# Kernel tuning notes

Measured on AMD Instinct MI355X. Metric: run time of the kernel, lower is better.

The kernel has to match this reference:

```python
import jax, jax.numpy as jnp
import numpy as np
import math

H, W = 1024, 1024

def setup_inputs() -> dict:
    key = jax.random.key(0)
    img = jax.random.uniform(key, (H, W), dtype=jnp.float32) * 255.0
    return {"InputImage": img}

def _phase_congruency(img):
    nrows, ncols = img.shape
    minWaveLength, mult = 3.0, 2.1
    nscale, norient = 5, 6
    sigmaOnf, k, cutOff, g = 0.55, 2.0, 0.5, 10.0
    eps = 1e-4

    cy, cx = nrows // 2, ncols // 2
    yy, xx = jnp.mgrid[0:nrows, 0:ncols]
    yy = (yy - cy) / nrows
    xx = (xx - cx) / ncols
    radius = jnp.sqrt(xx ** 2 + yy ** 2)
    radius = radius.at[cy, cx].set(1.0)
    theta = jnp.arctan2(-yy, xx)
    sintheta, costheta = jnp.sin(theta), jnp.cos(theta)

    # low-pass Butterworth (order 15, cutoff 0.45)
    normradius = radius / (jnp.abs(xx).max() * 2)
    lowpass = 1.0 / (1.0 + (normradius / 0.45) ** 30)

    # log-Gabor radial filters, [nscale, H, W]
    s = jnp.arange(nscale, dtype=jnp.float32)
    fo = 1.0 / (minWaveLength * mult ** s)            # [S]
    logGabor = jnp.exp(-jnp.log(radius[None] * (1.0 / fo)[:, None, None]) ** 2
                       / (2 * math.log(sigmaOnf) ** 2))
    annular = logGabor * lowpass[None]
    annular = annular.at[:, cy, cx].set(0.0)

    # angular spread, [norient, H, W]
    angl = jnp.arange(norient, dtype=jnp.float32) * (math.pi / norient)
    cosA, sinA = jnp.cos(angl), jnp.sin(angl)
    ds = sintheta[None] * cosA[:, None, None] - costheta[None] * sinA[:, None, None]
    dc = costheta[None] * cosA[:, None, None] + sintheta[None] * sinA[:, None, None]
    dtheta = jnp.minimum(jnp.abs(jnp.arctan2(ds, dc)) * (norient / 2), math.pi)
    spread = (jnp.cos(dtheta) + 1.0) / 2.0

    # full filter bank [O, S, H, W], shifted to DFT layout
    filt = jnp.fft.ifftshift(spread[:, None] * annular[None], axes=(-2, -1))

    F = jnp.fft.fft2(img)                              # complex64
    # cv2.idft is unscaled -> multiply numpy-style ifft by N
    z = jnp.fft.ifft2(filt * F[None, None]) * (nrows * ncols)   # [O,S,H,W]
    # original code: E (even) = channel 1 = Im(z), O (odd) = channel 0 = Re(z)
    E, O = z.imag, z.real
    An = jnp.abs(z)

    sumE = E.sum(axis=1)        # [O,H,W]
    sumO = O.sum(axis=1)
    sumAn = An.sum(axis=1)
    maxAn = An.max(axis=1)
    tau = jnp.median(An[:, 0].reshape(norient, -1), axis=1) / math.sqrt(math.log(4.0))

    XEnergy = jnp.sqrt(sumE ** 2 + sumO ** 2) + eps
    MeanE = sumE / XEnergy
    MeanO = sumO / XEnergy
    Energy = (E * MeanE[:, None] + O * MeanO[:, None]
              - jnp.abs(E * MeanO[:, None] - O * MeanE[:, None])).sum(axis=1)

    totalTau = tau * (1 - (1 / mult) ** nscale) / (1 - 1 / mult)   # [O]
    T = totalTau * math.sqrt(math.pi / 2) + k * totalTau * math.sqrt((4 - math.pi) / 2)
    Energy = jnp.maximum(Energy - T[:, None, None], 0.0)

    width = (sumAn / (maxAn + eps) - 1.0) / (nscale - 1)
    weight = 1.0 / (1.0 + jnp.exp((cutOff - width) * g))
    PC = weight * Energy / sumAn                       # [O,H,W]

    covx = PC * cosA[:, None, None]
    covy = PC * sinA[:, None, None]
    covx2 = (covx ** 2).sum(axis=0) / (norient / 2)
    covy2 = (covy ** 2).sum(axis=0) / (norient / 2)
    covxy = 4.0 * (covx * covy).sum(axis=0) / norient
    denom = jnp.sqrt(covxy ** 2 + (covx2 - covy2) ** 2) + eps
    M = (covy2 + covx2 + denom) / 2.0
    m = (covy2 + covx2 - denom) / 2.0
    return M, m

def reference(InputImage):
    M, m = _phase_congruency(InputImage)
    return (M, m)
```

## Files before the change

### kernel.cpp

```cpp
#include <hip/hip_runtime.h>
#include <math.h>

typedef float2 c2;

#define CSTR 1058
#define POS(n) (33*((n)>>5) + ((n)&31))

__device__ __forceinline__ c2 cmul(c2 a, c2 b){
  return make_float2(a.x*b.x - a.y*b.y, a.x*b.y + a.y*b.x);
}

__constant__ float2 c_tw32[16] = {
  {1.0f, 0.0f},
  {0.980785280f, 0.195090322f},
  {0.923879533f, 0.382683432f},
  {0.831469612f, 0.555570233f},
  {0.707106781f, 0.707106781f},
  {0.555570233f, 0.831469612f},
  {0.382683432f, 0.923879533f},
  {0.195090322f, 0.980785280f},
  {0.0f, 1.0f},
  {-0.195090322f, 0.980785280f},
  {-0.382683432f, 0.923879533f},
  {-0.555570233f, 0.831469612f},
  {-0.707106781f, 0.707106781f},
  {-0.831469612f, 0.555570233f},
  {-0.923879533f, 0.382683432f},
  {-0.980785280f, 0.195090322f}
};

__constant__ float c_lnfo[5]  = {1.0986123f, 1.8405496f, 2.5824700f, 3.3244106f, 4.0663219f};
__constant__ float c_angl[6]  = {0.0f, 0.5235988f, 1.0471976f, 1.5707963f, 2.0943951f, 2.6179939f};
__constant__ float c_cosA[6] = {1.0f, 0.8660254038f, 0.5f, 6.123233996e-17f, -0.5f, -0.8660254038f};
__constant__ float c_sinA[6] = {0.0f, 0.5f, 0.8660254038f, 1.0f, 0.8660254038f, 0.5f};

__device__ __forceinline__ constexpr int rev5(int k){
  return ((k&1)<<4) | ((k&2)<<2) | (k&4) | ((k&8)>>2) | ((k>>4)&1);
}

template<int SIGN, int M>
__device__ __forceinline__ void stage32(c2* r){
#pragma unroll
  for (int g = 0; g < 32; g += 2*M){
#pragma unroll
    for (int i = 0; i < M; ++i){
      const c2 a = r[g+i], b = r[g+i+M];
      r[g+i] = make_float2(a.x+b.x, a.y+b.y);
      c2 d = make_float2(a.x-b.x, a.y-b.y);
      if (i != 0){
        const float2 tt = c_tw32[i*(16/M)];
        d = cmul(d, make_float2(tt.x, (float)SIGN*tt.y));
      }
      r[g+i+M] = d;
    }
  }
}

template<int SIGN>
__device__ __forceinline__ void fft32(c2* r){
  stage32<SIGN,16>(r);
  stage32<SIGN,8>(r);
  stage32<SIGN,4>(r);
  stage32<SIGN,2>(r);
  stage32<SIGN,1>(r);
}

template<int SIGN>
__device__ void fft1024_4step(c2* slab, int t){
  const int sub = t & 7;
  const int idx = t >> 3;
  c2* line = slab + sub*CSTR;
  c2 r[32];
#pragma unroll
  for (int a = 0; a < 32; ++a) r[a] = line[33*a + idx];
  fft32<SIGN>(r);
  {
    const float ang = (float)SIGN * 0.006135923151542565f * (float)idx;
    c2 wst; sincosf(ang, &wst.y, &wst.x);
    c2 wc = make_float2(1.f, 0.f);
#pragma unroll
    for (int d = 0; d < 32; ++d){
      if ((d & 7) == 0 && d != 0){ float s, c; sincosf(ang*(float)d, &s, &c); wc = make_float2(c, s); }
      c2 v = r[rev5(d)];
      if (d != 0) v = cmul(v, wc);
      line[33*d + idx] = v;
      wc = cmul(wc, wst);
    }
  }
  __syncthreads();
#pragma unroll
  for (int b = 0; b < 32; ++b) r[b] = line[33*idx + b];
  __syncthreads();
  fft32<SIGN>(r);
#pragma unroll
  for (int c = 0; c < 32; ++c) line[33*c + idx] = r[rev5(c)];
}


template<int SIGN>
__global__ __launch_bounds__(256, 2) void k_col_fft(c2* __restrict__ Z){
  __shared__ c2 slab[8*CSTR];
  const int t = threadIdx.x;
  c2* base = Z + (size_t)blockIdx.y * 1048576;
  const int col0 = blockIdx.x * 8;
  const int cl = t & 7, rw = t >> 3;
#pragma unroll
  for (int it = 0; it < 32; ++it){
    const int row = it*32 + rw;
    slab[cl*CSTR + 33*it + rw] = base[(size_t)row*1024 + col0 + cl];
  }
  __syncthreads();
  fft1024_4step<SIGN>(slab, t);
  __syncthreads();
#pragma unroll
  for (int it = 0; it < 32; ++it){
    const int row = it*32 + rw;
    base[(size_t)row*1024 + col0 + cl] = slab[cl*CSTR + 33*it + rw];
  }
}

__global__ __launch_bounds__(256, 2) void k_row_fft_real(const float* __restrict__ in, c2* __restrict__ out){
  __shared__ c2 slab[8*CSTR];
  const int t = threadIdx.x;
  const int row0 = blockIdx.x * 8;
#pragma unroll
  for (int it = 0; it < 32; ++it){
    const int g = it*256 + t;
    const int r = g >> 10, n = g & 1023;
    slab[r*CSTR + POS(n)] = make_float2(in[(size_t)(row0+r)*1024 + n], 0.f);
  }
  __syncthreads();
  fft1024_4step<-1>(slab, t);
  __syncthreads();
#pragma unroll
  for (int it = 0; it < 32; ++it){
    const int g = it*256 + t;
    const int r = g >> 10, n = g & 1023;
    out[(size_t)(row0+r)*1024 + n] = slab[r*CSTR + POS(n)];
  }
}

__global__ __launch_bounds__(256, 2) void k_row_ifft_filter(const c2* __restrict__ F, c2* __restrict__ Z,
                                                            const float* __restrict__ lnrT,
                                                            const float* __restrict__ thetaT, int slot0){
  __shared__ c2 slab[8*CSTR];
  const int t = threadIdx.x;
  const int gslot = slot0 + blockIdx.y;
  const int orient = gslot / 5, scale = gslot - orient*5;
  const float lnfo = c_lnfo[scale], angl = c_angl[orient];
  const int row0 = blockIdx.x * 8;
  c2* dst = Z + (size_t)blockIdx.y * 1048576;
#pragma unroll
  for (int it = 0; it < 32; ++it){
    const int g = it*256 + t;
    const int r = g >> 10, n = g & 1023;
    const size_t gi = (size_t)(row0+r)*1024 + n;
    const c2 v = F[gi];
    const float lnr = lnrT[gi], th = thetaT[gi];
    const float u = lnr + lnfo;
    const float lg = __expf(-u*u*1.3989572f);
    const float lp = 1.0f/(1.0f + __expf(fmaf(30.f, lnr, 23.955231f)));
    float d = th - angl;
    if (d <= -3.14159274f) d += 6.28318548f;
    const float dth = fminf(fabsf(d)*3.0f, 3.14159274f);
    const float f = lg*lp*0.5f*(__cosf(dth)+1.0f);
    slab[r*CSTR + POS(n)] = make_float2(v.x*f, v.y*f);
  }
  __syncthreads();
  fft1024_4step<1>(slab, t);
  __syncthreads();
#pragma unroll
  for (int it = 0; it < 32; ++it){
    const int g = it*256 + t;
    const int r = g >> 10, n = g & 1023;
    dst[(size_t)(row0+r)*1024 + n] = slab[r*CSTR + POS(n)];
  }
}

__global__ __launch_bounds__(256) void k_filt_tab(float* __restrict__ lnrT, float* __restrict__ thetaT){
  const int r = blockIdx.x;
  const int t = threadIdx.x;
  const float yy = (float)(r < 512 ? r : r - 1024) * (1.0f/1024.0f);
#pragma unroll
  for (int j = 0; j < 4; ++j){
    const int c = t + 256*j;
    const float xx = (float)(c < 512 ? c : c - 1024) * (1.0f/1024.0f);
    const float radius = sqrtf(xx*xx + yy*yy);
    float lnr = logf(radius);
    if (r == 0 && c == 0) lnr = __int_as_float(0x7F800000);
    lnrT[r*1024 + c] = lnr;
    thetaT[r*1024 + c] = atan2f(-yy, xx);
  }
}


__device__ __forceinline__ unsigned amp_bits(const c2 v){
  return __float_as_uint(sqrtf(v.x*v.x + v.y*v.y));
}

__global__ __launch_bounds__(256) void k_med_p1b(const c2* __restrict__ Zb, size_t oStride,
                                                 unsigned* __restrict__ g1, int oBase){
  __shared__ unsigned h[4][4096];
  const int t = threadIdx.x;
  const int wv = t >> 6;
  const c2* z0 = Zb + (size_t)blockIdx.y * oStride;
  unsigned* gg = g1 + (size_t)(oBase + blockIdx.y) * 4096;
  for (int j = t; j < 4*4096; j += 256) ((unsigned*)h)[j] = 0;
  __syncthreads();
  const int base = blockIdx.x * 16384;
  for (int it = 0; it < 64; ++it){
    const unsigned bits = amp_bits(z0[base + it*256 + t]);
    atomicAdd(&h[wv][bits >> 20], 1u);
  }
  __syncthreads();
  for (int j = t; j < 4096; j += 256){
    const unsigned s = h[0][j] + h[1][j] + h[2][j] + h[3][j];
    if (s) atomicAdd(&gg[j], s);
  }
}

__global__ __launch_bounds__(256) void k_sel1b(const unsigned* __restrict__ g1,
                                               unsigned* __restrict__ sc1,
                                               unsigned* __restrict__ g2, int oBase){
  __shared__ unsigned partial[256];
  const int t = threadIdx.x;
  const int oo = oBase + blockIdx.x;
  const unsigned* gg = g1 + (size_t)oo * 4096;
  unsigned loc[16]; unsigned s = 0;
#pragma unroll
  for (int j = 0; j < 16; ++j){ loc[j] = gg[t*16 + j]; s += loc[j]; }
  partial[t] = s;
  __syncthreads();
  unsigned p = 0;
  for (int u = 0; u < t; ++u) p += partial[u];
  for (int which = 0; which < 2; ++which){
    const unsigned R = 524287u + (unsigned)which;
    if (R >= p && R - p < s){
      unsigned cum = p;
      for (int j = 0; j < 16; ++j){
        if (R - cum < loc[j]){ sc1[oo*4 + which*2] = (unsigned)(t*16 + j); sc1[oo*4 + which*2+1] = R - cum; break; }
        cum += loc[j];
      }
    }
  }
  for (int j = t; j < 8192; j += 256) g2[(size_t)oo*8192 + j] = 0;
}

__global__ __launch_bounds__(256) void k_med_p2b(const c2* __restrict__ Zb, size_t oStride,
                                                 const unsigned* __restrict__ sc1,
                                                 unsigned* __restrict__ g2, int oBase){
  __shared__ unsigned h[2][4096];
  const int t = threadIdx.x;
  const int oo = oBase + blockIdx.y;
  const c2* z0 = Zb + (size_t)blockIdx.y * oStride;
  unsigned* gg = g2 + (size_t)oo * 8192;
  for (int j = t; j < 8192; j += 256) ((unsigned*)h)[j] = 0;
  __syncthreads();
  const unsigned b0 = sc1[oo*4 + 0], b1 = sc1[oo*4 + 2];
  const int base = blockIdx.x * 16384;
  for (int it = 0; it < 64; ++it){
    const unsigned bits = amp_bits(z0[base + it*256 + t]);
    const unsigned top = bits >> 20;
    const unsigned mid = (bits >> 8) & 4095u;
    if (top == b0)      atomicAdd(&h[0][mid], 1u);
    else if (top == b1) atomicAdd(&h[1][mid], 1u);
  }
  __syncthreads();
  for (int j = t; j < 4096; j += 256){
    if (h[0][j]) atomicAdd(&gg[j], h[0][j]);
    if (h[1][j]) atomicAdd(&gg[4096 + j], h[1][j]);
  }
}

__global__ __launch_bounds__(256) void k_sel2b(const unsigned* __restrict__ g2,
                                               const unsigned* __restrict__ sc1,
                                               unsigned* __restrict__ sc2,
                                               unsigned* __restrict__ g3, int oBase){
  __shared__ unsigned partial[256];
  const int t = threadIdx.x;
  const int oo = oBase + blockIdx.x;
  const unsigned b0 = sc1[oo*4+0], lr0 = sc1[oo*4+1], b1 = sc1[oo*4+2], lr1 = sc1[oo*4+3];
  for (int which = 0; which < 2; ++which){
    const unsigned* hh = g2 + (size_t)oo*8192 + ((which == 1 && b1 != b0) ? 4096 : 0);
    const unsigned R = which ? lr1 : lr0;
    unsigned loc[16]; unsigned s = 0;
#pragma unroll
    for (int j = 0; j < 16; ++j){ loc[j] = hh[t*16 + j]; s += loc[j]; }
    partial[t] = s;
    __syncthreads();
    unsigned p = 0;
    for (int u = 0; u < t; ++u) p += partial[u];
    if (R >= p && R - p < s){
      unsigned cum = p;
      for (int j = 0; j < 16; ++j){
        if (R - cum < loc[j]){ sc2[oo*4 + which*2] = (unsigned)(t*16 + j); sc2[oo*4 + which*2+1] = R - cum; break; }
        cum += loc[j];
      }
    }
    __syncthreads();
  }
  for (int j = t; j < 512; j += 256) g3[(size_t)oo*512 + j] = 0;
}

__global__ __launch_bounds__(256) void k_med_p3b(const c2* __restrict__ Zb, size_t oStride,
                                                 const unsigned* __restrict__ sc1,
                                                 const unsigned* __restrict__ sc2,
                                                 unsigned* __restrict__ g3, int oBase){
  __shared__ unsigned h[2][256];
  const int t = threadIdx.x;
  const int oo = oBase + blockIdx.y;
  const c2* z0 = Zb + (size_t)blockIdx.y * oStride;
  unsigned* gg = g3 + (size_t)oo * 512;
  h[0][t] = 0; h[1][t] = 0;
  __syncthreads();
  const unsigned k0 = (sc1[oo*4+0] << 12) | sc2[oo*4+0];
  const unsigned k1 = (sc1[oo*4+2] << 12) | sc2[oo*4+2];
  const int base = blockIdx.x * 16384;
  for (int it = 0; it < 64; ++it){
    const unsigned bits = amp_bits(z0[base + it*256 + t]);
    const unsigned key = bits >> 8;
    if (key == k0)       atomicAdd(&h[0][bits & 255u], 1u);
    else if (key == k1)  atomicAdd(&h[1][bits & 255u], 1u);
  }
  __syncthreads();
  if (h[0][t]) atomicAdd(&gg[t], h[0][t]);
  if (h[1][t]) atomicAdd(&gg[256 + t], h[1][t]);
}

__global__ __launch_bounds__(256) void k_sel3b(const unsigned* __restrict__ g3,
                                               const unsigned* __restrict__ sc1,
                                               const unsigned* __restrict__ sc2,
                                               float* __restrict__ Tval, int oBase){
  __shared__ unsigned partial[256];
  __shared__ float vres[2];
  const int t = threadIdx.x;
  const int oo = oBase + blockIdx.x;
  const unsigned k0 = (sc1[oo*4+0] << 12) | sc2[oo*4+0];
  const unsigned k1 = (sc1[oo*4+2] << 12) | sc2[oo*4+2];
  for (int which = 0; which < 2; ++which){
    const unsigned* hh = g3 + (size_t)oo*512 + ((which == 1 && k1 != k0) ? 256 : 0);
    const unsigned R = which ? sc2[oo*4+3] : sc2[oo*4+1];
    partial[t] = hh[t];
    __syncthreads();
    unsigned p = 0;
    for (int u = 0; u < t; ++u) p += partial[u];
    if (R >= p && R - p < partial[t]){
      const unsigned key = which ? k1 : k0;
      vres[which] = __uint_as_float((key << 8) | (unsigned)t);
    }
    __syncthreads();
  }
  if (t == 0){
    const float med = 0.5f * (vres[0] + vres[1]);
    const float tau = med / 1.17741001f;
    const float totalTau = tau * 1.8623464f;
    const float T = totalTau * 1.25331414f + 2.0f * totalTau * 0.65513638f;
    Tval[oo] = T;
  }
}


__global__ __launch_bounds__(256) void k_pix_all(const c2* __restrict__ Z, const float* __restrict__ Tval,
                                                 float* __restrict__ out){
  const int i = blockIdx.x * 256 + threadIdx.x;
  float covx2 = 0.f, covy2 = 0.f, covxy = 0.f;
#pragma unroll
  for (int o = 0; o < 6; ++o){
    const float T = Tval[o];
    float E[5], O[5];
    float sumE = 0.f, sumO = 0.f, sumAn = 0.f, maxAn = 0.f;
#pragma unroll
    for (int s = 0; s < 5; ++s){
      const c2 z = Z[(size_t)(o*5 + s) * 1048576 + i];
      O[s] = z.x; E[s] = z.y;
      const float an = sqrtf(z.x*z.x + z.y*z.y);
      sumE += E[s]; sumO += O[s]; sumAn += an; maxAn = fmaxf(maxAn, an);
    }
    const float XE = sqrtf(sumE*sumE + sumO*sumO) + 1e-4f;
    const float ME = sumE / XE, MO = sumO / XE;
    float energy = 0.f;
#pragma unroll
    for (int s = 0; s < 5; ++s)
      energy += E[s]*ME + O[s]*MO - fabsf(E[s]*MO - O[s]*ME);
    energy = fmaxf(energy - T, 0.f);
    const float width = (sumAn / (maxAn + 1e-4f) - 1.0f) * 0.25f;
    const float weight = 1.0f / (1.0f + expf((0.5f - width) * 10.0f));
    const float PC = weight * energy / sumAn;
    const float cx = PC * c_cosA[o], cy = PC * c_sinA[o];
    covx2 += cx*cx; covy2 += cy*cy; covxy += cx*cy;
  }
  covx2 *= (1.0f/3.0f);
  covy2 *= (1.0f/3.0f);
  covxy *= (4.0f/6.0f);
  const float dnm = sqrtf(covxy*covxy + (covx2 - covy2)*(covx2 - covy2)) + 1e-4f;
  const float ss = covy2 + covx2;
  out[i] = (ss + dnm) / 2.0f;
  out[1048576 + i] = (ss - dnm) / 2.0f;
}


__global__ __launch_bounds__(256) void k_pix(const c2* __restrict__ Z, const float* __restrict__ Tp,
                                             float cA, float sA,
                                             float* __restrict__ ax2, float* __restrict__ ay2,
                                             float* __restrict__ axy, int first){
  const int i = blockIdx.x * 256 + threadIdx.x;
  const float T = *Tp;
  float E[5], O[5];
  float sumE = 0.f, sumO = 0.f, sumAn = 0.f, maxAn = 0.f;
#pragma unroll
  for (int s = 0; s < 5; ++s){
    const c2 z = Z[(size_t)s * 1048576 + i];
    O[s] = z.x; E[s] = z.y;
    const float an = sqrtf(z.x*z.x + z.y*z.y);
    sumE += E[s]; sumO += O[s]; sumAn += an; maxAn = fmaxf(maxAn, an);
  }
  const float XE = sqrtf(sumE*sumE + sumO*sumO) + 1e-4f;
  const float ME = sumE / XE, MO = sumO / XE;
  float energy = 0.f;
#pragma unroll
  for (int s = 0; s < 5; ++s)
    energy += E[s]*ME + O[s]*MO - fabsf(E[s]*MO - O[s]*ME);
  energy = fmaxf(energy - T, 0.f);
  const float width = (sumAn / (maxAn + 1e-4f) - 1.0f) * 0.25f;
  const float weight = 1.0f / (1.0f + expf((0.5f - width) * 10.0f));
  const float PC = weight * energy / sumAn;
  const float cx = PC * cA, cy = PC * sA;
  if (first){ ax2[i] = cx*cx; ay2[i] = cy*cy; axy[i] = cx*cy; }
  else      { ax2[i] += cx*cx; ay2[i] += cy*cy; axy[i] += cx*cy; }
}

__global__ __launch_bounds__(256) void k_final(const float* __restrict__ ax2, const float* __restrict__ ay2,
                                               const float* __restrict__ axy, float* __restrict__ out){
  const int i = blockIdx.x * 256 + threadIdx.x;
  const float cx2 = ax2[i] / 3.0f;
  const float cy2 = ay2[i] / 3.0f;
  const float cxy = 4.0f * axy[i] / 6.0f;
  const float dnm = sqrtf(cxy*cxy + (cx2 - cy2)*(cx2 - cy2)) + 1e-4f;
  const float ss = cy2 + cx2;
  out[i] = (ss + dnm) / 2.0f;
  out[1048576 + i] = (ss - dnm) / 2.0f;
}

extern "C" void kernel_launch(void* const* d_in, const int* in_sizes, int n_in,
                              void* d_out, int out_size, void* d_ws, size_t ws_size,
                              hipStream_t stream){
  (void)in_sizes; (void)n_in; (void)out_size;
  const float* img = (const float*)d_in[0];
  float* out = (float*)d_out;
  char* w = (char*)d_ws;

  const dim3 th(256);

  if (ws_size >= (size_t)268435456){
    c2* F  = (c2*)(w);
    c2* Z  = (c2*)(w + 8388608);
    float* lnrT   = (float*)(w + 260046848);
    float* thetaT = (float*)(w + 264241152);
    unsigned* g1  = (unsigned*)(w);
    unsigned* g2  = (unsigned*)(w + 98304);
    unsigned* g3  = (unsigned*)(w + 294912);
    unsigned* sc1 = (unsigned*)(w + 307200);
    unsigned* sc2 = (unsigned*)(w + 307328);
    float* Tval   = (float*)(w + 307456);

    k_filt_tab<<<dim3(1024), th, 0, stream>>>(lnrT, thetaT);

    k_row_fft_real<<<dim3(128), th, 0, stream>>>(img, F);
    k_col_fft<-1><<<dim3(128, 1), th, 0, stream>>>(F);

    k_row_ifft_filter<<<dim3(128, 30), th, 0, stream>>>(F, Z, lnrT, thetaT, 0);
    k_col_fft<1><<<dim3(128, 30), th, 0, stream>>>(Z);

    hipMemsetAsync(g1, 0, 6*16384, stream);
    const size_t oStride = (size_t)5 * 1048576;
    k_med_p1b<<<dim3(64, 6), th, 0, stream>>>(Z, oStride, g1, 0);
    k_sel1b<<<dim3(6), th, 0, stream>>>(g1, sc1, g2, 0);
    k_med_p2b<<<dim3(64, 6), th, 0, stream>>>(Z, oStride, sc1, g2, 0);
    k_sel2b<<<dim3(6), th, 0, stream>>>(g2, sc1, sc2, g3, 0);
    k_med_p3b<<<dim3(64, 6), th, 0, stream>>>(Z, oStride, sc1, sc2, g3, 0);
    k_sel3b<<<dim3(6), th, 0, stream>>>(g3, sc1, sc2, Tval, 0);

    k_pix_all<<<dim3(4096), th, 0, stream>>>(Z, Tval, out);
  } else {
    c2* F   = (c2*)(w);
    c2* C5  = (c2*)(w + 8388608);
    float* lnrT   = (float*)(w + 50331648);
    float* thetaT = (float*)(w + 54525952);
    float* ax2 = (float*)(w + 58720256);
    float* ay2 = ax2 + 1048576;
    float* axy = ay2 + 1048576;
    unsigned* g1  = (unsigned*)(w + 71303168);
    unsigned* g2  = (unsigned*)(w + 71319552);
    unsigned* g3  = (unsigned*)(w + 71352320);
    unsigned* sc1 = (unsigned*)(w + 71354368);
    unsigned* sc2 = (unsigned*)(w + 71354496);
    float* Tval   = (float*)(w + 71354624);

    k_filt_tab<<<dim3(1024), th, 0, stream>>>(lnrT, thetaT);
    k_row_fft_real<<<dim3(128), th, 0, stream>>>(img, F);
    k_col_fft<-1><<<dim3(128, 1), th, 0, stream>>>(F);

    for (int o = 0; o < 6; ++o){
      k_row_ifft_filter<<<dim3(128, 5), th, 0, stream>>>(F, C5, lnrT, thetaT, o*5);
      k_col_fft<1><<<dim3(128, 5), th, 0, stream>>>(C5);

      hipMemsetAsync(g1, 0, 16384, stream);
      k_med_p1b<<<dim3(64, 1), th, 0, stream>>>(C5, 0, g1, 0);
      k_sel1b<<<dim3(1), th, 0, stream>>>(g1, sc1, g2, 0);
      k_med_p2b<<<dim3(64, 1), th, 0, stream>>>(C5, 0, sc1, g2, 0);
      k_sel2b<<<dim3(1), th, 0, stream>>>(g2, sc1, sc2, g3, 0);
      k_med_p3b<<<dim3(64, 1), th, 0, stream>>>(C5, 0, sc1, sc2, g3, 0);
      k_sel3b<<<dim3(1), th, 0, stream>>>(g3, sc1, sc2, Tval, 0);

      const double a = (double)o * (M_PI/6.0);
      k_pix<<<dim3(4096), th, 0, stream>>>(C5, Tval, (float)cos(a), (float)sin(a),
                                           ax2, ay2, axy, (o == 0) ? 1 : 0);
    }
    k_final<<<dim3(4096), th, 0, stream>>>(ax2, ay2, axy, out);
  }
}
```

Before: 460.4 us.

## Load FFT inputs directly into registers and skip LDS staging

The row FFT, filtered inverse row FFT and column FFT kernels now read their data straight from global memory into per-thread registers and run the first radix-32 pass immediately. After the second pass they write results straight back to global memory. Shared memory is used only for the middle twiddle-and-transpose step. This removes two full LDS round trips and two barriers per transform. In exchange, the row kernels now read and write global memory in 64-byte pieces spread across 8 rows instead of fully contiguous rows, which lowers coalescing efficiency.

```diff
diff --git a/kernel.cpp b/kernel.cpp
--- a/kernel.cpp
+++ b/kernel.cpp
@@ -4,7 +4,6 @@
 typedef float2 c2;
 
 #define CSTR 1058
-#define POS(n) (33*((n)>>5) + ((n)&31))
 
 __device__ __forceinline__ c2 cmul(c2 a, c2 b){
   return make_float2(a.x*b.x - a.y*b.y, a.x*b.y + a.y*b.x);
@@ -66,34 +65,22 @@
 }
 
 template<int SIGN>
-__device__ void fft1024_4step(c2* slab, int t){
-  const int sub = t & 7;
-  const int idx = t >> 3;
-  c2* line = slab + sub*CSTR;
-  c2 r[32];
-#pragma unroll
-  for (int a = 0; a < 32; ++a) r[a] = line[33*a + idx];
+__device__ __forceinline__ void fourstep_mid(c2* r, c2* line, int idx){
+  const float ang = (float)SIGN * 0.006135923151542565f * (float)idx;
+  c2 wst; sincosf(ang, &wst.y, &wst.x);
+  c2 wc = make_float2(1.f, 0.f);
+#pragma unroll
+  for (int d = 0; d < 32; ++d){
+    if ((d & 7) == 0 && d != 0){ float s, c; sincosf(ang*(float)d, &s, &c); wc = make_float2(c, s); }
+    c2 v = r[rev5(d)];
+    if (d != 0) v = cmul(v, wc);
+    line[33*d + idx] = v;
+    wc = cmul(wc, wst);
+  }
+  __syncthreads();
+#pragma unroll
+  for (int b = 0; b < 32; ++b) r[b] = line[33*idx + b];
   fft32<SIGN>(r);
-  {
-    const float ang = (float)SIGN * 0.006135923151542565f * (float)idx;
-    c2 wst; sincosf(ang, &wst.y, &wst.x);
-    c2 wc = make_float2(1.f, 0.f);
-#pragma unroll
-    for (int d = 0; d < 32; ++d){
-      if ((d & 7) == 0 && d != 0){ float s, c; sincosf(ang*(float)d, &s, &c); wc = make_float2(c, s); }
-      c2 v = r[rev5(d)];
-      if (d != 0) v = cmul(v, wc);
-      line[33*d + idx] = v;
-      wc = cmul(wc, wst);
-    }
-  }
-  __syncthreads();
-#pragma unroll
-  for (int b = 0; b < 32; ++b) r[b] = line[33*idx + b];
-  __syncthreads();
-  fft32<SIGN>(r);
-#pragma unroll
-  for (int c = 0; c < 32; ++c) line[33*c + idx] = r[rev5(c)];
 }
 
 
@@ -102,42 +89,35 @@
   __shared__ c2 slab[8*CSTR];
   const int t = threadIdx.x;
   c2* base = Z + (size_t)blockIdx.y * 1048576;
-  const int col0 = blockIdx.x * 8;
-  const int cl = t & 7, rw = t >> 3;
-#pragma unroll
-  for (int it = 0; it < 32; ++it){
-    const int row = it*32 + rw;
-    slab[cl*CSTR + 33*it + rw] = base[(size_t)row*1024 + col0 + cl];
-  }
-  __syncthreads();
-  fft1024_4step<SIGN>(slab, t);
-  __syncthreads();
-#pragma unroll
-  for (int it = 0; it < 32; ++it){
-    const int row = it*32 + rw;
-    base[(size_t)row*1024 + col0 + cl] = slab[cl*CSTR + 33*it + rw];
-  }
+  const int sub = t & 7, idx = t >> 3;
+  const int col = blockIdx.x*8 + sub;
+  c2 r[32];
+#pragma unroll
+  for (int a = 0; a < 32; ++a)
+    r[a] = base[(size_t)(32*a + idx)*1024 + col];
+  fft32<SIGN>(r);
+  fourstep_mid<SIGN>(r, slab + sub*CSTR, idx);
+#pragma unroll
+  for (int c = 0; c < 32; ++c)
+    base[(size_t)(32*c + idx)*1024 + col] = r[rev5(c)];
 }
 
 __global__ __launch_bounds__(256, 2) void k_row_fft_real(const float* __restrict__ in, c2* __restrict__ out){
   __shared__ c2 slab[8*CSTR];
   const int t = threadIdx.x;
-  const int row0 = blockIdx.x * 8;
-#pragma unroll
-  for (int it = 0; it < 32; ++it){
-    const int g = it*256 + t;
-    const int r = g >> 10, n = g & 1023;
-    slab[r*CSTR + POS(n)] = make_float2(in[(size_t)(row0+r)*1024 + n], 0.f);
-  }
-  __syncthreads();
-  fft1024_4step<-1>(slab, t);
-  __syncthreads();
-#pragma unroll
-  for (int it = 0; it < 32; ++it){
-    const int g = it*256 + t;
-    const int r = g >> 10, n = g & 1023;
-    out[(size_t)(row0+r)*1024 + n] = slab[r*CSTR + POS(n)];
-  }
+  const int sub = t & 7, idx = t >> 3;
+  const int row = blockIdx.x*8 + sub;
+  const float* src = in + (size_t)row * 1024;
+  c2* dst = out + (size_t)row * 1024;
+  c2 r[32];
+#pragma unroll
+  for (int a = 0; a < 32; ++a)
+    r[a] = make_float2(src[32*a + idx], 0.f);
+  fft32<-1>(r);
+  fourstep_mid<-1>(r, slab + sub*CSTR, idx);
+#pragma unroll
+  for (int c = 0; c < 32; ++c)
+    dst[32*c + idx] = r[rev5(c)];
 }
 
 __global__ __launch_bounds__(256, 2) void k_row_ifft_filter(const c2* __restrict__ F, c2* __restrict__ Z,
@@ -145,18 +125,21 @@
                                                             const float* __restrict__ thetaT, int slot0){
   __shared__ c2 slab[8*CSTR];
   const int t = threadIdx.x;
+  const int sub = t & 7, idx = t >> 3;
   const int gslot = slot0 + blockIdx.y;
   const int orient = gslot / 5, scale = gslot - orient*5;
   const float lnfo = c_lnfo[scale], angl = c_angl[orient];
-  const int row0 = blockIdx.x * 8;
-  c2* dst = Z + (size_t)blockIdx.y * 1048576;
-#pragma unroll
-  for (int it = 0; it < 32; ++it){
-    const int g = it*256 + t;
-    const int r = g >> 10, n = g & 1023;
-    const size_t gi = (size_t)(row0+r)*1024 + n;
-    const c2 v = F[gi];
-    const float lnr = lnrT[gi], th = thetaT[gi];
+  const int row = blockIdx.x*8 + sub;
+  const c2* src = F + (size_t)row * 1024;
+  const float* lnrR = lnrT + (size_t)row * 1024;
+  const float* thR  = thetaT + (size_t)row * 1024;
+  c2* dst = Z + (size_t)blockIdx.y * 1048576 + (size_t)row * 1024;
+  c2 r[32];
+#pragma unroll
+  for (int a = 0; a < 32; ++a){
+    const int n = 32*a + idx;
+    const c2 v = src[n];
+    const float lnr = lnrR[n], th = thR[n];
     const float u = lnr + lnfo;
     const float lg = __expf(-u*u*1.3989572f);
     const float lp = 1.0f/(1.0f + __expf(fmaf(30.f, lnr, 23.955231f)));
@@ -164,17 +147,13 @@
     if (d <= -3.14159274f) d += 6.28318548f;
     const float dth = fminf(fabsf(d)*3.0f, 3.14159274f);
     const float f = lg*lp*0.5f*(__cosf(dth)+1.0f);
-    slab[r*CSTR + POS(n)] = make_float2(v.x*f, v.y*f);
-  }
-  __syncthreads();
-  fft1024_4step<1>(slab, t);
-  __syncthreads();
-#pragma unroll
-  for (int it = 0; it < 32; ++it){
-    const int g = it*256 + t;
-    const int r = g >> 10, n = g & 1023;
-    dst[(size_t)(row0+r)*1024 + n] = slab[r*CSTR + POS(n)];
-  }
+    r[a] = make_float2(v.x*f, v.y*f);
+  }
+  fft32<1>(r);
+  fourstep_mid<1>(r, slab + sub*CSTR, idx);
+#pragma unroll
+  for (int c = 0; c < 32; ++c)
+    dst[32*c + idx] = r[rev5(c)];
 }
 
 __global__ __launch_bounds__(256) void k_filt_tab(float* __restrict__ lnrT, float* __restrict__ thetaT){
```

After: 469.4 us. No clear change (+2.0%).
